# Optimization experiments

Hardware: AMD Instinct MI355X
Metric: run time of the kernel (lower is better)

## Reference

```python
import jax, jax.numpy as jnp
import numpy as np
from jax import lax

LAYER_NUM = 6
EPS = 1e-9
BN_EPS = 1e-5

# CNOT ring on 3 qubits: CNOT(0,1), CNOT(1,2), CNOT(2,0); qubit 0 = MSB.
_P = np.zeros((8, 8), np.float32)
for _b in range(8):
    b0, b1, b2 = (_b >> 2) & 1, (_b >> 1) & 1, _b & 1
    b1 ^= b0
    b2 ^= b1
    b0 ^= b2
    _P[(b0 << 2) | (b1 << 1) | b2, _b] = 1.0
CNOT_RING = jnp.asarray(_P)


def _ry(t):
    c, s = jnp.cos(t / 2), jnp.sin(t / 2)
    return jnp.stack([jnp.stack([c, -s]), jnp.stack([s, c])])


def _channel_unitary(wc):
    # wc: [layer_num, 3] rotation angles -> full 8x8 circuit unitary (real, RY+CNOT)
    U = jnp.eye(8, dtype=wc.dtype)
    for l in range(wc.shape[0]):
        K = jnp.kron(jnp.kron(_ry(wc[l, 0]), _ry(wc[l, 1])), _ry(wc[l, 2]))
        U = CNOT_RING @ K @ U
    return U


def qcnn(x, weights, out_dim, out_size):
    # x: [B, C, H, W]; weights: [C, layer_num, 3]; 2x2 kernel, stride 2, no padding
    B, C, H, W = x.shape
    OH, OW = H // 2, W // 2
    # im2col: [B, C*4, OH, OW] with feature dim ordered (C, kh, kw)
    patches = lax.conv_general_dilated_patches(x, (2, 2), (2, 2), 'VALID')
    patches = patches.reshape(B, C, 4, OH * OW).transpose(0, 1, 3, 2)  # [B,C,P,4]
    # amplitude embedding on 2 data qubits, ancilla (MSB) in |0>
    nrm = jnp.linalg.norm(patches, axis=-1, keepdims=True)
    amp = patches / jnp.maximum(nrm, EPS)
    psi0 = jnp.pad(amp, ((0, 0), (0, 0), (0, 0), (0, 4)))  # [B,C,P,8]
    U = jax.vmap(_channel_unitary)(weights)  # [C,8,8]
    psi = jnp.einsum('cjk,bcpk->bcpj', U, psi0)
    probs = psi * psi
    data = probs[..., :4]  # post-select ancilla = 0
    data = data / jnp.maximum(data.sum(-1, keepdims=True), EPS)
    return data.reshape(B, out_dim, out_size, out_size)


def batchnorm2d(x, gamma, beta):
    mean = x.mean(axis=(0, 2, 3), keepdims=True)
    var = x.var(axis=(0, 2, 3), keepdims=True)
    xn = (x - mean) * lax.rsqrt(var + BN_EPS)
    return xn * gamma[None, :, None, None] + beta[None, :, None, None]


def setup_inputs() -> dict:
    key = jax.random.key(0)
    ks = jax.random.split(key, 5)
    return {
        'z': jax.random.normal(ks[0], (1024, 256, 4, 4), jnp.float32),
        'w1': jax.random.normal(ks[1], (256, LAYER_NUM, 3), jnp.float32),
        'w2': jax.random.normal(ks[2], (64, LAYER_NUM, 3), jnp.float32),
        'w3': jax.random.normal(ks[3], (16, LAYER_NUM, 3), jnp.float32),
        'w4': jax.random.normal(ks[4], (4, LAYER_NUM, 3), jnp.float32),
        'gamma2': jnp.ones((64,), jnp.float32), 'beta2': jnp.zeros((64,), jnp.float32),
        'gamma3': jnp.ones((16,), jnp.float32), 'beta3': jnp.zeros((16,), jnp.float32),
        'gamma4': jnp.ones((4,), jnp.float32), 'beta4': jnp.zeros((4,), jnp.float32),
        'gamma_f': jnp.ones((1,), jnp.float32), 'beta_f': jnp.zeros((1,), jnp.float32),
    }


def reference(z, w1, w2, w3, w4, gamma2, beta2, gamma3, beta3, gamma4, beta4, gamma_f, beta_f):
    s1 = qcnn(z, w1, 64, 8)
    x = jax.nn.relu(batchnorm2d(s1, gamma2, beta2))
    s2 = qcnn(x, w2, 16, 16)
    x = jax.nn.relu(batchnorm2d(s2, gamma3, beta3))
    s3 = qcnn(x, w3, 4, 32)
    x = jax.nn.relu(batchnorm2d(s3, gamma4, beta4))
    s4 = qcnn(x, w4, 1, 64)
    s4_bn = batchnorm2d(s4, gamma_f, beta_f)
    return jnp.tanh(s4_bn), s4, s4_bn
```

## Files before the change

### kernel.cpp

```cpp
#include <hip/hip_runtime.h>
#include <math.h>


#define NB 1024

__global__ __launch_bounds__(256) void build_V_kernel(
    const float* __restrict__ w1, const float* __restrict__ w2,
    const float* __restrict__ w3, const float* __restrict__ w4,
    float* __restrict__ V)
{
    int t = blockIdx.x * blockDim.x + threadIdx.x;
    if (t >= 340) return;
    const float* w; float* vout;
    if (t < 256)      { w = w1 + t*18;        vout = V + t*16; }
    else if (t < 320) { w = w2 + (t-256)*18;  vout = V + 4096 + (t-256)*16; }
    else if (t < 336) { w = w3 + (t-320)*18;  vout = V + 5120 + (t-320)*16; }
    else              { w = w4 + (t-336)*18;  vout = V + 5376 + (t-336)*16; }
    const int perm[8] = {0,5,7,2,3,6,4,1};
    float U[8][8];
    #pragma unroll
    for (int i=0;i<8;i++)
        #pragma unroll
        for (int j=0;j<8;j++) U[i][j] = (i==j) ? 1.0f : 0.0f;
    for (int l=0;l<6;l++){
        float c0 = cosf(0.5f*w[l*3+0]), s0 = sinf(0.5f*w[l*3+0]);
        float c1 = cosf(0.5f*w[l*3+1]), s1 = sinf(0.5f*w[l*3+1]);
        float c2 = cosf(0.5f*w[l*3+2]), s2 = sinf(0.5f*w[l*3+2]);
        #pragma unroll
        for (int col=0; col<8; col++){
            float v[8];
            #pragma unroll
            for (int r=0;r<8;r++) v[r] = U[r][col];
            #pragma unroll
            for (int b=0;b<8;b+=2){ float x=v[b], y=v[b+1]; v[b]=c2*x-s2*y; v[b+1]=s2*x+c2*y; }
            #pragma unroll
            for (int g=0;g<8;g+=4)
                #pragma unroll
                for (int i=0;i<2;i++){ int a=g+i, b=g+i+2; float x=v[a], y=v[b]; v[a]=c1*x-s1*y; v[b]=s1*x+c1*y; }
            #pragma unroll
            for (int i=0;i<4;i++){ float x=v[i], y=v[i+4]; v[i]=c0*x-s0*y; v[i+4]=s0*x+c0*y; }
            #pragma unroll
            for (int r=0;r<8;r++) U[perm[r]][col] = v[r];
        }
    }
    #pragma unroll
    for (int j=0;j<4;j++)
        #pragma unroll
        for (int k=0;k<4;k++) vout[j*4+k] = U[j][k];
}

template<int C, int H, int W, bool BN>
__global__ __launch_bounds__(256) void qcnn_kernel(
    const float* __restrict__ x, const float* __restrict__ V,
    const float* __restrict__ scale, const float* __restrict__ shift,
    float* __restrict__ out, float* __restrict__ psum, float* __restrict__ pssq)
{
    constexpr int HW  = H*W;
    constexpr int P   = HW/4;
    constexpr int OW  = W/2;
    constexpr int LP  = (P==4)?2:(P==16)?4:(P==64)?6:8;
    constexpr int LOW = (OW==2)?1:(OW==4)?2:(OW==8)?3:4;
    constexpr int OC  = C/4;
    constexpr int CPB = 256/P;
    constexpr int OCB = (CPB/4) < 1 ? 1 : (CPB/4);
    constexpr int DIV = OC/OCB;
    constexpr int NSLOT = NB/DIV;
    constexpr int G   = (4*P < 64) ? 4*P : 64;

    __shared__ float sBin[2*OCB];
    if (threadIdx.x < 2*OCB) sBin[threadIdx.x] = 0.0f;
    __syncthreads();

    const int r0  = (blockIdx.x & 3) * 256;
    const int oc0 = r0 >> (LP+2);

    for (int it=0; it<4; ++it){
        int tid = (it<<18) + (blockIdx.x<<8) + threadIdx.x;
        int b  = tid >> 10;
        int r  = tid & 1023;
        int c  = r >> LP;
        int p  = r & (P-1);
        int oh = p >> LOW;
        int ow = p & (OW-1);
        const float* xb = x + ((size_t)b<<12) + c*HW + (oh*2)*W + (ow*2);
        float2 t0 = *reinterpret_cast<const float2*>(xb);
        float2 t1 = *reinterpret_cast<const float2*>(xb + W);
        float x0=t0.x, x1=t0.y, x2=t1.x, x3=t1.y;
        if constexpr (BN){
            float sc = scale[c], sh = shift[c];
            x0 = fmaxf(x0*sc+sh, 0.0f);
            x1 = fmaxf(x1*sc+sh, 0.0f);
            x2 = fmaxf(x2*sc+sh, 0.0f);
            x3 = fmaxf(x3*sc+sh, 0.0f);
        }
        float nrm = sqrtf(x0*x0 + x1*x1 + x2*x2 + x3*x3);
        float inv = 1.0f / fmaxf(nrm, 1e-9f);
        float a0=x0*inv, a1=x1*inv, a2=x2*inv, a3=x3*inv;
        const float4* Vc = reinterpret_cast<const float4*>(V + c*16);
        float4 v0 = Vc[0], v1 = Vc[1], v2 = Vc[2], v3 = Vc[3];
        float q0 = v0.x*a0 + v0.y*a1 + v0.z*a2 + v0.w*a3;
        float q1 = v1.x*a0 + v1.y*a1 + v1.z*a2 + v1.w*a3;
        float q2 = v2.x*a0 + v2.y*a1 + v2.z*a2 + v2.w*a3;
        float q3 = v3.x*a0 + v3.y*a1 + v3.z*a2 + v3.w*a3;
        q0*=q0; q1*=q1; q2*=q2; q3*=q3;
        float s = q0+q1+q2+q3;
        float dinv = 1.0f / fmaxf(s, 1e-9f);
        float d0=q0*dinv, d1=q1*dinv, d2=q2*dinv, d3=q3*dinv;
        *reinterpret_cast<float4*>(out + ((size_t)b<<12) + c*HW + (p<<2)) =
            make_float4(d0,d1,d2,d3);
        float ls  = d0+d1+d2+d3;
        float lss = d0*d0 + d1*d1 + d2*d2 + d3*d3;
        #pragma unroll
        for (int off=1; off<G; off<<=1){ ls += __shfl_xor(ls, off); lss += __shfl_xor(lss, off); }
        if ((threadIdx.x & (G-1)) == 0){
            int ocl = (r >> (LP+2)) - oc0;
            atomicAdd(&sBin[ocl], ls);
            atomicAdd(&sBin[OCB + ocl], lss);
        }
    }
    __syncthreads();
    if (threadIdx.x < OCB){
        int slot = blockIdx.x / DIV;
        psum[(oc0 + threadIdx.x)*NSLOT + slot] = sBin[threadIdx.x];
        pssq[(oc0 + threadIdx.x)*NSLOT + slot] = sBin[OCB + threadIdx.x];
    }
}

__global__ __launch_bounds__(256) void stats_kernel(
    const float* __restrict__ psum, const float* __restrict__ pssq,
    const float* __restrict__ gamma, const float* __restrict__ beta,
    float* __restrict__ scale, float* __restrict__ shift,
    int nslot, float invN)
{
    __shared__ float sh[8];
    int oc = blockIdx.x;
    float s=0.0f, ss=0.0f;
    for (int i=threadIdx.x; i<nslot; i+=256){ s += psum[oc*nslot+i]; ss += pssq[oc*nslot+i]; }
    #pragma unroll
    for (int off=32; off; off>>=1){ s += __shfl_down(s, off); ss += __shfl_down(ss, off); }
    int wid = threadIdx.x >> 6, lane = threadIdx.x & 63;
    if (lane==0){ sh[wid]=s; sh[4+wid]=ss; }
    __syncthreads();
    if (threadIdx.x==0){
        s  = sh[0]+sh[1]+sh[2]+sh[3];
        ss = sh[4]+sh[5]+sh[6]+sh[7];
        float mean = s*invN;
        float var  = ss*invN - mean*mean;
        float rinv = 1.0f / sqrtf(var + 1e-5f);
        float sc = gamma[oc]*rinv;
        scale[oc] = sc;
        shift[oc] = beta[oc] - mean*sc;
    }
}

__global__ __launch_bounds__(256) void final_kernel(
    const float* __restrict__ s4, const float* __restrict__ sc_p,
    const float* __restrict__ sh_p, float* __restrict__ out_tanh,
    float* __restrict__ out_bn)
{
    float sc = sc_p[0], sh = sh_p[0];
    int i = blockIdx.x*blockDim.x + threadIdx.x;
    float4 v = reinterpret_cast<const float4*>(s4)[i];
    float4 bn = make_float4(v.x*sc+sh, v.y*sc+sh, v.z*sc+sh, v.w*sc+sh);
    reinterpret_cast<float4*>(out_bn)[i] = bn;
    reinterpret_cast<float4*>(out_tanh)[i] =
        make_float4(tanhf(bn.x), tanhf(bn.y), tanhf(bn.z), tanhf(bn.w));
}

extern "C" void kernel_launch(void* const* d_in, const int* in_sizes, int n_in,
                              void* d_out, int out_size, void* d_ws, size_t ws_size,
                              hipStream_t stream)
{
    const float* z      = (const float*)d_in[0];
    const float* w1     = (const float*)d_in[1];
    const float* w2     = (const float*)d_in[2];
    const float* w3     = (const float*)d_in[3];
    const float* w4     = (const float*)d_in[4];
    const float* gamma2 = (const float*)d_in[5];
    const float* beta2  = (const float*)d_in[6];
    const float* gamma3 = (const float*)d_in[7];
    const float* beta3  = (const float*)d_in[8];
    const float* gamma4 = (const float*)d_in[9];
    const float* beta4  = (const float*)d_in[10];
    const float* gammaf = (const float*)d_in[11];
    const float* betaf  = (const float*)d_in[12];
    float* out = (float*)d_out;
    float* ws  = (float*)d_ws;

    float* V      = ws;
    float* scale2 = ws + 5504;  float* shift2 = ws + 5568;
    float* scale3 = ws + 5632;  float* shift3 = ws + 5696;
    float* scale4 = ws + 5760;  float* shift4 = ws + 5824;
    float* scalef = ws + 5888;  float* shiftf = ws + 5952;
    float* ps1 = ws + 6144;   float* pq1 = ws + 22528;
    float* ps2 = ws + 38912;  float* pq2 = ws + 43008;
    float* ps3 = ws + 47104;  float* pq3 = ws + 48128;
    float* ps4 = ws + 49152;  float* pq4 = ws + 50176;
    float* bufA = ws + 65536;
    float* bufB = ws + 65536 + 4194304;
    float* s4   = out + 4194304;
    float* s4bn = out + 8388608;

    build_V_kernel<<<2, 256, 0, stream>>>(w1, w2, w3, w4, V);

    qcnn_kernel<256,4,4,false><<<NB, 256, 0, stream>>>(z, V, nullptr, nullptr, bufA, ps1, pq1);
    stats_kernel<<<64, 256, 0, stream>>>(ps1, pq1, gamma2, beta2, scale2, shift2, 256, 1.0f/65536.0f);

    qcnn_kernel<64,8,8,true><<<NB, 256, 0, stream>>>(bufA, V+4096, scale2, shift2, bufB, ps2, pq2);
    stats_kernel<<<16, 256, 0, stream>>>(ps2, pq2, gamma3, beta3, scale3, shift3, 256, 1.0f/262144.0f);

    qcnn_kernel<16,16,16,true><<<NB, 256, 0, stream>>>(bufB, V+5120, scale3, shift3, bufA, ps3, pq3);
    stats_kernel<<<4, 256, 0, stream>>>(ps3, pq3, gamma4, beta4, scale4, shift4, 256, 1.0f/1048576.0f);

    qcnn_kernel<4,32,32,true><<<NB, 256, 0, stream>>>(bufA, V+5376, scale4, shift4, s4, ps4, pq4);
    stats_kernel<<<1, 256, 0, stream>>>(ps4, pq4, gammaf, betaf, scalef, shiftf, 1024, 1.0f/4194304.0f);

    final_kernel<<<4096, 256, 0, stream>>>(s4, scalef, shiftf, out, s4bn);
}
```

Measured before the change: 146.9 us.

## Fuse all QCNN layers into one cooperative kernel with per-image LDS residency

Replaces the nine separate layer, stats and final launches with a single cooperative kernel. Each block keeps one 4096-float image in shared memory across all four layers, and grid.sync handles the global batchnorm statistics. Per-block partial sums are reduced with atomics into 8 banked global accumulators instead of slot arrays plus stats kernels. This removes intermediate global round-trips and launch gaps, but adds four grid-wide barriers and needs all 1024 blocks (16KB LDS each) to be co-resident.

```diff
diff --git a/kernel.cpp b/kernel.cpp
--- a/kernel.cpp
+++ b/kernel.cpp
@@ -1,15 +1,18 @@
 #include <hip/hip_runtime.h>
+#include <hip/hip_cooperative_groups.h>
 #include <math.h>
 
-
-#define NB 1024
+namespace cg = cooperative_groups;
+
 
 __global__ __launch_bounds__(256) void build_V_kernel(
     const float* __restrict__ w1, const float* __restrict__ w2,
     const float* __restrict__ w3, const float* __restrict__ w4,
-    float* __restrict__ V)
+    float* __restrict__ V, float* __restrict__ acc)
 {
     int t = blockIdx.x * blockDim.x + threadIdx.x;
+    int j = t - 512;
+    if (j >= 0 && j < 1360) acc[j] = 0.0f;
     if (t >= 340) return;
     const float* w; float* vout;
     if (t < 256)      { w = w1 + t*18;        vout = V + t*16; }
@@ -21,7 +24,7 @@
     #pragma unroll
     for (int i=0;i<8;i++)
         #pragma unroll
-        for (int j=0;j<8;j++) U[i][j] = (i==j) ? 1.0f : 0.0f;
+        for (int jj=0;jj<8;jj++) U[i][jj] = (i==jj) ? 1.0f : 0.0f;
     for (int l=0;l<6;l++){
         float c0 = cosf(0.5f*w[l*3+0]), s0 = sinf(0.5f*w[l*3+0]);
         float c1 = cosf(0.5f*w[l*3+1]), s1 = sinf(0.5f*w[l*3+1]);
@@ -32,11 +35,11 @@
             #pragma unroll
             for (int r=0;r<8;r++) v[r] = U[r][col];
             #pragma unroll
-            for (int b=0;b<8;b+=2){ float x=v[b], y=v[b+1]; v[b]=c2*x-s2*y; v[b+1]=s2*x+c2*y; }
+            for (int bb=0;bb<8;bb+=2){ float x=v[bb], y=v[bb+1]; v[bb]=c2*x-s2*y; v[bb+1]=s2*x+c2*y; }
             #pragma unroll
             for (int g=0;g<8;g+=4)
                 #pragma unroll
-                for (int i=0;i<2;i++){ int a=g+i, b=g+i+2; float x=v[a], y=v[b]; v[a]=c1*x-s1*y; v[b]=s1*x+c1*y; }
+                for (int i=0;i<2;i++){ int a=g+i, bq=g+i+2; float x=v[a], y=v[bq]; v[a]=c1*x-s1*y; v[bq]=s1*x+c1*y; }
             #pragma unroll
             for (int i=0;i<4;i++){ float x=v[i], y=v[i+4]; v[i]=c0*x-s0*y; v[i+4]=s0*x+c0*y; }
             #pragma unroll
@@ -44,127 +47,177 @@
         }
     }
     #pragma unroll
-    for (int j=0;j<4;j++)
-        #pragma unroll
-        for (int k=0;k<4;k++) vout[j*4+k] = U[j][k];
+    for (int jj=0;jj<4;jj++)
+        #pragma unroll
+        for (int k=0;k<4;k++) vout[jj*4+k] = U[jj][k];
 }
 
 template<int C, int H, int W, bool BN>
-__global__ __launch_bounds__(256) void qcnn_kernel(
-    const float* __restrict__ x, const float* __restrict__ V,
-    const float* __restrict__ scale, const float* __restrict__ shift,
-    float* __restrict__ out, float* __restrict__ psum, float* __restrict__ pssq)
+__device__ __forceinline__ void layer_step(
+    float* __restrict__ data, const float* __restrict__ Vg,
+    const float* __restrict__ sSc, const float* __restrict__ sSh,
+    float* __restrict__ sbin, float* __restrict__ accL, int bank,
+    float* __restrict__ gout, int b)
 {
     constexpr int HW  = H*W;
     constexpr int P   = HW/4;
     constexpr int OW  = W/2;
+    constexpr int OC  = C/4;
     constexpr int LP  = (P==4)?2:(P==16)?4:(P==64)?6:8;
     constexpr int LOW = (OW==2)?1:(OW==4)?2:(OW==8)?3:4;
-    constexpr int OC  = C/4;
-    constexpr int CPB = 256/P;
-    constexpr int OCB = (CPB/4) < 1 ? 1 : (CPB/4);
-    constexpr int DIV = OC/OCB;
-    constexpr int NSLOT = NB/DIV;
-    constexpr int G   = (4*P < 64) ? 4*P : 64;
-
-    __shared__ float sBin[2*OCB];
-    if (threadIdx.x < 2*OCB) sBin[threadIdx.x] = 0.0f;
-    __syncthreads();
-
-    const int r0  = (blockIdx.x & 3) * 256;
-    const int oc0 = r0 >> (LP+2);
-
-    for (int it=0; it<4; ++it){
-        int tid = (it<<18) + (blockIdx.x<<8) + threadIdx.x;
-        int b  = tid >> 10;
-        int r  = tid & 1023;
-        int c  = r >> LP;
-        int p  = r & (P-1);
-        int oh = p >> LOW;
-        int ow = p & (OW-1);
-        const float* xb = x + ((size_t)b<<12) + c*HW + (oh*2)*W + (ow*2);
-        float2 t0 = *reinterpret_cast<const float2*>(xb);
-        float2 t1 = *reinterpret_cast<const float2*>(xb + W);
-        float x0=t0.x, x1=t0.y, x2=t1.x, x3=t1.y;
+    constexpr int RED = ((1<<(LP+2)) < 64) ? (1<<(LP+2)) : 64;
+    const int tid = threadIdx.x;
+
+    if (tid < 2*OC) sbin[tid] = 0.0f;
+    __syncthreads();
+
+    float xv[4][4];
+    #pragma unroll
+    for (int k=0;k<4;k++){
+        int u = tid + 256*k;
+        int c = u >> LP, p = u & (P-1);
+        int oh = p >> LOW, ow = p & (OW-1);
+        int base = c*HW + (oh*2)*W + (ow*2);
+        float x0 = data[base], x1 = data[base+1];
+        float x2 = data[base+W], x3 = data[base+W+1];
         if constexpr (BN){
-            float sc = scale[c], sh = shift[c];
-            x0 = fmaxf(x0*sc+sh, 0.0f);
-            x1 = fmaxf(x1*sc+sh, 0.0f);
-            x2 = fmaxf(x2*sc+sh, 0.0f);
-            x3 = fmaxf(x3*sc+sh, 0.0f);
-        }
+            float sc = sSc[c], sh = sSh[c];
+            x0 = fmaxf(fmaf(x0,sc,sh), 0.0f);
+            x1 = fmaxf(fmaf(x1,sc,sh), 0.0f);
+            x2 = fmaxf(fmaf(x2,sc,sh), 0.0f);
+            x3 = fmaxf(fmaf(x3,sc,sh), 0.0f);
+        }
+        xv[k][0]=x0; xv[k][1]=x1; xv[k][2]=x2; xv[k][3]=x3;
+    }
+    __syncthreads();
+
+    #pragma unroll
+    for (int k=0;k<4;k++){
+        int u = tid + 256*k;
+        int c = u >> LP, p = u & (P-1);
+        float x0=xv[k][0], x1=xv[k][1], x2=xv[k][2], x3=xv[k][3];
         float nrm = sqrtf(x0*x0 + x1*x1 + x2*x2 + x3*x3);
         float inv = 1.0f / fmaxf(nrm, 1e-9f);
         float a0=x0*inv, a1=x1*inv, a2=x2*inv, a3=x3*inv;
-        const float4* Vc = reinterpret_cast<const float4*>(V + c*16);
+        const float4* Vc = reinterpret_cast<const float4*>(Vg + (c<<4));
         float4 v0 = Vc[0], v1 = Vc[1], v2 = Vc[2], v3 = Vc[3];
         float q0 = v0.x*a0 + v0.y*a1 + v0.z*a2 + v0.w*a3;
         float q1 = v1.x*a0 + v1.y*a1 + v1.z*a2 + v1.w*a3;
         float q2 = v2.x*a0 + v2.y*a1 + v2.z*a2 + v2.w*a3;
         float q3 = v3.x*a0 + v3.y*a1 + v3.z*a2 + v3.w*a3;
         q0*=q0; q1*=q1; q2*=q2; q3*=q3;
-        float s = q0+q1+q2+q3;
-        float dinv = 1.0f / fmaxf(s, 1e-9f);
+        float dinv = 1.0f / fmaxf(q0+q1+q2+q3, 1e-9f);
         float d0=q0*dinv, d1=q1*dinv, d2=q2*dinv, d3=q3*dinv;
-        *reinterpret_cast<float4*>(out + ((size_t)b<<12) + c*HW + (p<<2)) =
-            make_float4(d0,d1,d2,d3);
+        float4 o4 = make_float4(d0,d1,d2,d3);
+        reinterpret_cast<float4*>(data)[c*P + p] = o4;
+        if (gout)
+            reinterpret_cast<float4*>(gout)[(size_t)b*1024 + u] = o4;
         float ls  = d0+d1+d2+d3;
         float lss = d0*d0 + d1*d1 + d2*d2 + d3*d3;
         #pragma unroll
-        for (int off=1; off<G; off<<=1){ ls += __shfl_xor(ls, off); lss += __shfl_xor(lss, off); }
-        if ((threadIdx.x & (G-1)) == 0){
-            int ocl = (r >> (LP+2)) - oc0;
-            atomicAdd(&sBin[ocl], ls);
-            atomicAdd(&sBin[OCB + ocl], lss);
-        }
-    }
-    __syncthreads();
-    if (threadIdx.x < OCB){
-        int slot = blockIdx.x / DIV;
-        psum[(oc0 + threadIdx.x)*NSLOT + slot] = sBin[threadIdx.x];
-        pssq[(oc0 + threadIdx.x)*NSLOT + slot] = sBin[OCB + threadIdx.x];
-    }
-}
-
-__global__ __launch_bounds__(256) void stats_kernel(
-    const float* __restrict__ psum, const float* __restrict__ pssq,
+        for (int off=1; off<RED; off<<=1){
+            ls  += __shfl_xor(ls,  off);
+            lss += __shfl_xor(lss, off);
+        }
+        if ((tid & (RED-1)) == 0){
+            int oc = u >> (LP+2);
+            atomicAdd(&sbin[oc],      ls);
+            atomicAdd(&sbin[OC + oc], lss);
+        }
+    }
+    __syncthreads();
+
+    if (tid < OC){
+        atomicAdd(&accL[bank*2*OC + tid],      sbin[tid]);
+        atomicAdd(&accL[bank*2*OC + OC + tid], sbin[OC + tid]);
+    }
+}
+
+template<int OC>
+__device__ __forceinline__ void bn_params(
+    const float* __restrict__ accL,
     const float* __restrict__ gamma, const float* __restrict__ beta,
-    float* __restrict__ scale, float* __restrict__ shift,
-    int nslot, float invN)
-{
-    __shared__ float sh[8];
-    int oc = blockIdx.x;
-    float s=0.0f, ss=0.0f;
-    for (int i=threadIdx.x; i<nslot; i+=256){ s += psum[oc*nslot+i]; ss += pssq[oc*nslot+i]; }
-    #pragma unroll
-    for (int off=32; off; off>>=1){ s += __shfl_down(s, off); ss += __shfl_down(ss, off); }
-    int wid = threadIdx.x >> 6, lane = threadIdx.x & 63;
-    if (lane==0){ sh[wid]=s; sh[4+wid]=ss; }
-    __syncthreads();
-    if (threadIdx.x==0){
-        s  = sh[0]+sh[1]+sh[2]+sh[3];
-        ss = sh[4]+sh[5]+sh[6]+sh[7];
+    float invN, float* __restrict__ sSc, float* __restrict__ sSh, int tid)
+{
+    if (tid < OC){
+        float s=0.0f, q=0.0f;
+        #pragma unroll
+        for (int bk=0;bk<8;bk++){
+            s += accL[bk*2*OC + tid];
+            q += accL[bk*2*OC + OC + tid];
+        }
         float mean = s*invN;
-        float var  = ss*invN - mean*mean;
-        float rinv = 1.0f / sqrtf(var + 1e-5f);
-        float sc = gamma[oc]*rinv;
-        scale[oc] = sc;
-        shift[oc] = beta[oc] - mean*sc;
-    }
-}
-
-__global__ __launch_bounds__(256) void final_kernel(
-    const float* __restrict__ s4, const float* __restrict__ sc_p,
-    const float* __restrict__ sh_p, float* __restrict__ out_tanh,
+        float var  = q*invN - mean*mean;
+        float r    = 1.0f / sqrtf(var + 1e-5f);
+        float sc   = gamma[tid]*r;
+        sSc[tid] = sc;
+        sSh[tid] = beta[tid] - mean*sc;
+    }
+    __syncthreads();
+}
+
+__global__ __launch_bounds__(256, 4) void fused_kernel(
+    const float* __restrict__ z, const float* __restrict__ V,
+    float* __restrict__ acc,
+    const float* __restrict__ g2, const float* __restrict__ b2,
+    const float* __restrict__ g3, const float* __restrict__ b3,
+    const float* __restrict__ g4, const float* __restrict__ b4,
+    const float* __restrict__ gf, const float* __restrict__ bf,
+    float* __restrict__ out_tanh, float* __restrict__ out_s4,
     float* __restrict__ out_bn)
 {
-    float sc = sc_p[0], sh = sh_p[0];
-    int i = blockIdx.x*blockDim.x + threadIdx.x;
-    float4 v = reinterpret_cast<const float4*>(s4)[i];
-    float4 bn = make_float4(v.x*sc+sh, v.y*sc+sh, v.z*sc+sh, v.w*sc+sh);
-    reinterpret_cast<float4*>(out_bn)[i] = bn;
-    reinterpret_cast<float4*>(out_tanh)[i] =
-        make_float4(tanhf(bn.x), tanhf(bn.y), tanhf(bn.z), tanhf(bn.w));
+    __shared__ __align__(16) float data[4096];
+    __shared__ float sbin[128];
+    __shared__ float sSc[64], sSh[64];
+    const int tid  = threadIdx.x;
+    const int b    = blockIdx.x;
+    const int bank = b & 7;
+    cg::grid_group grid = cg::this_grid();
+
+    float* acc1 = acc;
+    float* acc2 = acc + 1024;
+    float* acc3 = acc + 1280;
+    float* acc4 = acc + 1344;
+
+    const float4* zb = reinterpret_cast<const float4*>(z) + (size_t)b*1024;
+    float4* dv = reinterpret_cast<float4*>(data);
+    #pragma unroll
+    for (int k=0;k<4;k++) dv[k*256+tid] = zb[k*256+tid];
+
+    layer_step<256,4,4,false>(data, V,      nullptr, nullptr, sbin, acc1, bank, nullptr, b);
+    grid.sync();
+    bn_params<64>(acc1, g2, b2, 1.0f/65536.0f,   sSc, sSh, tid);
+
+    layer_step<64,8,8,true>(data, V+4096, sSc, sSh, sbin, acc2, bank, nullptr, b);
+    grid.sync();
+    bn_params<16>(acc2, g3, b3, 1.0f/262144.0f,  sSc, sSh, tid);
+
+    layer_step<16,16,16,true>(data, V+5120, sSc, sSh, sbin, acc3, bank, nullptr, b);
+    grid.sync();
+    bn_params<4>(acc3, g4, b4, 1.0f/1048576.0f,  sSc, sSh, tid);
+
+    layer_step<4,32,32,true>(data, V+5376, sSc, sSh, sbin, acc4, bank, out_s4, b);
+    grid.sync();
+
+    float s=0.0f, q=0.0f;
+    #pragma unroll
+    for (int bk=0;bk<8;bk++){ s += acc4[bk*2]; q += acc4[bk*2+1]; }
+    float mean = s*(1.0f/4194304.0f);
+    float var  = q*(1.0f/4194304.0f) - mean*mean;
+    float r    = 1.0f / sqrtf(var + 1e-5f);
+    float sc   = gf[0]*r;
+    float sh   = bf[0] - mean*sc;
+    float4* ot = reinterpret_cast<float4*>(out_tanh) + (size_t)b*1024;
+    float4* ob = reinterpret_cast<float4*>(out_bn)   + (size_t)b*1024;
+    #pragma unroll
+    for (int k=0;k<4;k++){
+        float4 v = dv[k*256+tid];
+        float4 bnv = make_float4(fmaf(v.x,sc,sh), fmaf(v.y,sc,sh),
+                                 fmaf(v.z,sc,sh), fmaf(v.w,sc,sh));
+        ob[k*256+tid] = bnv;
+        ot[k*256+tid] = make_float4(tanhf(bnv.x), tanhf(bnv.y),
+                                    tanhf(bnv.z), tanhf(bnv.w));
+    }
 }
 
 extern "C" void kernel_launch(void* const* d_in, const int* in_sizes, int n_in,
@@ -187,33 +240,23 @@
     float* out = (float*)d_out;
     float* ws  = (float*)d_ws;
 
-    float* V      = ws;
-    float* scale2 = ws + 5504;  float* shift2 = ws + 5568;
-    float* scale3 = ws + 5632;  float* shift3 = ws + 5696;
-    float* scale4 = ws + 5760;  float* shift4 = ws + 5824;
-    float* scalef = ws + 5888;  float* shiftf = ws + 5952;
-    float* ps1 = ws + 6144;   float* pq1 = ws + 22528;
-    float* ps2 = ws + 38912;  float* pq2 = ws + 43008;
-    float* ps3 = ws + 47104;  float* pq3 = ws + 48128;
-    float* ps4 = ws + 49152;  float* pq4 = ws + 50176;
-    float* bufA = ws + 65536;
-    float* bufB = ws + 65536 + 4194304;
-    float* s4   = out + 4194304;
-    float* s4bn = out + 8388608;
-
-    build_V_kernel<<<2, 256, 0, stream>>>(w1, w2, w3, w4, V);
-
-    qcnn_kernel<256,4,4,false><<<NB, 256, 0, stream>>>(z, V, nullptr, nullptr, bufA, ps1, pq1);
-    stats_kernel<<<64, 256, 0, stream>>>(ps1, pq1, gamma2, beta2, scale2, shift2, 256, 1.0f/65536.0f);
-
-    qcnn_kernel<64,8,8,true><<<NB, 256, 0, stream>>>(bufA, V+4096, scale2, shift2, bufB, ps2, pq2);
-    stats_kernel<<<16, 256, 0, stream>>>(ps2, pq2, gamma3, beta3, scale3, shift3, 256, 1.0f/262144.0f);
-
-    qcnn_kernel<16,16,16,true><<<NB, 256, 0, stream>>>(bufB, V+5120, scale3, shift3, bufA, ps3, pq3);
-    stats_kernel<<<4, 256, 0, stream>>>(ps3, pq3, gamma4, beta4, scale4, shift4, 256, 1.0f/1048576.0f);
-
-    qcnn_kernel<4,32,32,true><<<NB, 256, 0, stream>>>(bufA, V+5376, scale4, shift4, s4, ps4, pq4);
-    stats_kernel<<<1, 256, 0, stream>>>(ps4, pq4, gammaf, betaf, scalef, shiftf, 1024, 1.0f/4194304.0f);
-
-    final_kernel<<<4096, 256, 0, stream>>>(s4, scalef, shiftf, out, s4bn);
-}
+    float* V   = ws;
+    float* acc = ws + 8192;
+
+    float* out_tanh = out;
+    float* out_s4   = out + 4194304;
+    float* out_bn   = out + 8388608;
+
+    build_V_kernel<<<8, 256, 0, stream>>>(w1, w2, w3, w4, V, acc);
+
+    void* args[] = {
+        (void*)&z, (void*)&V, (void*)&acc,
+        (void*)&gamma2, (void*)&beta2,
+        (void*)&gamma3, (void*)&beta3,
+        (void*)&gamma4, (void*)&beta4,
+        (void*)&gammaf, (void*)&betaf,
+        (void*)&out_tanh, (void*)&out_s4, (void*)&out_bn
+    };
+    hipLaunchCooperativeKernel((const void*)fused_kernel,
+                               dim3(1024), dim3(256), args, 0, stream);
+}
```

Result: slower. 576.1 us (+292.1%).

## Fuse BN stats reduction into qcnn kernels via banked global atomics

Applied to the files above, without the earlier changes.

Removes the four separate stats kernels. Each qcnn block now atomically adds its per-channel partial sums into one of 8 global banks. The next layer's kernel reduces the banks and computes BN scale and shift into shared memory in its prologue, and the final kernel does the same for the last layer. This cuts four kernel launches and the partial-buffer traffic, at the cost of global atomics and redundant per-block stats computation. The accumulators are zeroed in build_V, so build_V must launch with enough blocks to cover them.

```diff
diff --git a/kernel.cpp b/kernel.cpp
--- a/kernel.cpp
+++ b/kernel.cpp
@@ -7,9 +7,11 @@
 __global__ __launch_bounds__(256) void build_V_kernel(
     const float* __restrict__ w1, const float* __restrict__ w2,
     const float* __restrict__ w3, const float* __restrict__ w4,
-    float* __restrict__ V)
+    float* __restrict__ V, float* __restrict__ acc)
 {
     int t = blockIdx.x * blockDim.x + threadIdx.x;
+    int j = t - 512;
+    if (j >= 0 && j < 1360) acc[j] = 0.0f;
     if (t >= 340) return;
     const float* w; float* vout;
     if (t < 256)      { w = w1 + t*18;        vout = V + t*16; }
@@ -21,7 +23,7 @@
     #pragma unroll
     for (int i=0;i<8;i++)
         #pragma unroll
-        for (int j=0;j<8;j++) U[i][j] = (i==j) ? 1.0f : 0.0f;
+        for (int jj=0;jj<8;jj++) U[i][jj] = (i==jj) ? 1.0f : 0.0f;
     for (int l=0;l<6;l++){
         float c0 = cosf(0.5f*w[l*3+0]), s0 = sinf(0.5f*w[l*3+0]);
         float c1 = cosf(0.5f*w[l*3+1]), s1 = sinf(0.5f*w[l*3+1]);
@@ -32,11 +34,11 @@
             #pragma unroll
             for (int r=0;r<8;r++) v[r] = U[r][col];
             #pragma unroll
-            for (int b=0;b<8;b+=2){ float x=v[b], y=v[b+1]; v[b]=c2*x-s2*y; v[b+1]=s2*x+c2*y; }
+            for (int bb=0;bb<8;bb+=2){ float x=v[bb], y=v[bb+1]; v[bb]=c2*x-s2*y; v[bb+1]=s2*x+c2*y; }
             #pragma unroll
             for (int g=0;g<8;g+=4)
                 #pragma unroll
-                for (int i=0;i<2;i++){ int a=g+i, b=g+i+2; float x=v[a], y=v[b]; v[a]=c1*x-s1*y; v[b]=s1*x+c1*y; }
+                for (int i=0;i<2;i++){ int a=g+i, bq=g+i+2; float x=v[a], y=v[bq]; v[a]=c1*x-s1*y; v[bq]=s1*x+c1*y; }
             #pragma unroll
             for (int i=0;i<4;i++){ float x=v[i], y=v[i+4]; v[i]=c0*x-s0*y; v[i+4]=s0*x+c0*y; }
             #pragma unroll
@@ -44,16 +46,17 @@
         }
     }
     #pragma unroll
-    for (int j=0;j<4;j++)
-        #pragma unroll
-        for (int k=0;k<4;k++) vout[j*4+k] = U[j][k];
+    for (int jj=0;jj<4;jj++)
+        #pragma unroll
+        for (int k=0;k<4;k++) vout[jj*4+k] = U[jj][k];
 }
 
 template<int C, int H, int W, bool BN>
 __global__ __launch_bounds__(256) void qcnn_kernel(
     const float* __restrict__ x, const float* __restrict__ V,
-    const float* __restrict__ scale, const float* __restrict__ shift,
-    float* __restrict__ out, float* __restrict__ psum, float* __restrict__ pssq)
+    const float* __restrict__ accPrev, const float* __restrict__ gamma,
+    const float* __restrict__ beta, float invN,
+    float* __restrict__ out, float* __restrict__ accOut)
 {
     constexpr int HW  = H*W;
     constexpr int P   = HW/4;
@@ -61,23 +64,39 @@
     constexpr int LP  = (P==4)?2:(P==16)?4:(P==64)?6:8;
     constexpr int LOW = (OW==2)?1:(OW==4)?2:(OW==8)?3:4;
     constexpr int OC  = C/4;
-    constexpr int CPB = 256/P;
-    constexpr int OCB = (CPB/4) < 1 ? 1 : (CPB/4);
-    constexpr int DIV = OC/OCB;
-    constexpr int NSLOT = NB/DIV;
+    constexpr int OCB = (64/P) < 1 ? 1 : (64/P);
     constexpr int G   = (4*P < 64) ? 4*P : 64;
 
     __shared__ float sBin[2*OCB];
-    if (threadIdx.x < 2*OCB) sBin[threadIdx.x] = 0.0f;
+    __shared__ float sSc[C], sSh[C];
+    const int tid = threadIdx.x;
+
+    if (tid < 2*OCB) sBin[tid] = 0.0f;
+    if constexpr (BN){
+        if (tid < C){
+            float s=0.0f, q=0.0f;
+            #pragma unroll
+            for (int bk=0;bk<8;bk++){
+                s += accPrev[bk*2*C + tid];
+                q += accPrev[bk*2*C + C + tid];
+            }
+            float mean = s*invN;
+            float var  = q*invN - mean*mean;
+            float r    = 1.0f / sqrtf(var + 1e-5f);
+            float sc   = gamma[tid]*r;
+            sSc[tid] = sc;
+            sSh[tid] = beta[tid] - mean*sc;
+        }
+    }
     __syncthreads();
 
     const int r0  = (blockIdx.x & 3) * 256;
     const int oc0 = r0 >> (LP+2);
 
     for (int it=0; it<4; ++it){
-        int tid = (it<<18) + (blockIdx.x<<8) + threadIdx.x;
-        int b  = tid >> 10;
-        int r  = tid & 1023;
+        int tg = (it<<18) + (blockIdx.x<<8) + tid;
+        int b  = tg >> 10;
+        int r  = tg & 1023;
         int c  = r >> LP;
         int p  = r & (P-1);
         int oh = p >> LOW;
@@ -87,81 +106,70 @@
         float2 t1 = *reinterpret_cast<const float2*>(xb + W);
         float x0=t0.x, x1=t0.y, x2=t1.x, x3=t1.y;
         if constexpr (BN){
-            float sc = scale[c], sh = shift[c];
-            x0 = fmaxf(x0*sc+sh, 0.0f);
-            x1 = fmaxf(x1*sc+sh, 0.0f);
-            x2 = fmaxf(x2*sc+sh, 0.0f);
-            x3 = fmaxf(x3*sc+sh, 0.0f);
+            float sc = sSc[c], sh = sSh[c];
+            x0 = fmaxf(fmaf(x0,sc,sh), 0.0f);
+            x1 = fmaxf(fmaf(x1,sc,sh), 0.0f);
+            x2 = fmaxf(fmaf(x2,sc,sh), 0.0f);
+            x3 = fmaxf(fmaf(x3,sc,sh), 0.0f);
         }
         float nrm = sqrtf(x0*x0 + x1*x1 + x2*x2 + x3*x3);
         float inv = 1.0f / fmaxf(nrm, 1e-9f);
         float a0=x0*inv, a1=x1*inv, a2=x2*inv, a3=x3*inv;
-        const float4* Vc = reinterpret_cast<const float4*>(V + c*16);
+        const float4* Vc = reinterpret_cast<const float4*>(V + (c<<4));
         float4 v0 = Vc[0], v1 = Vc[1], v2 = Vc[2], v3 = Vc[3];
         float q0 = v0.x*a0 + v0.y*a1 + v0.z*a2 + v0.w*a3;
         float q1 = v1.x*a0 + v1.y*a1 + v1.z*a2 + v1.w*a3;
         float q2 = v2.x*a0 + v2.y*a1 + v2.z*a2 + v2.w*a3;
         float q3 = v3.x*a0 + v3.y*a1 + v3.z*a2 + v3.w*a3;
         q0*=q0; q1*=q1; q2*=q2; q3*=q3;
-        float s = q0+q1+q2+q3;
-        float dinv = 1.0f / fmaxf(s, 1e-9f);
+        float dinv = 1.0f / fmaxf(q0+q1+q2+q3, 1e-9f);
         float d0=q0*dinv, d1=q1*dinv, d2=q2*dinv, d3=q3*dinv;
-        *reinterpret_cast<float4*>(out + ((size_t)b<<12) + c*HW + (p<<2)) =
+        *reinterpret_cast<float4*>(out + ((size_t)b<<12) + (r<<2)) =
             make_float4(d0,d1,d2,d3);
         float ls  = d0+d1+d2+d3;
         float lss = d0*d0 + d1*d1 + d2*d2 + d3*d3;
         #pragma unroll
-        for (int off=1; off<G; off<<=1){ ls += __shfl_xor(ls, off); lss += __shfl_xor(lss, off); }
-        if ((threadIdx.x & (G-1)) == 0){
+        for (int off=1; off<G; off<<=1){
+            ls  += __shfl_xor(ls,  off);
+            lss += __shfl_xor(lss, off);
+        }
+        if ((tid & (G-1)) == 0){
             int ocl = (r >> (LP+2)) - oc0;
             atomicAdd(&sBin[ocl], ls);
             atomicAdd(&sBin[OCB + ocl], lss);
         }
     }
     __syncthreads();
-    if (threadIdx.x < OCB){
-        int slot = blockIdx.x / DIV;
-        psum[(oc0 + threadIdx.x)*NSLOT + slot] = sBin[threadIdx.x];
-        pssq[(oc0 + threadIdx.x)*NSLOT + slot] = sBin[OCB + threadIdx.x];
-    }
-}
-
-__global__ __launch_bounds__(256) void stats_kernel(
-    const float* __restrict__ psum, const float* __restrict__ pssq,
-    const float* __restrict__ gamma, const float* __restrict__ beta,
-    float* __restrict__ scale, float* __restrict__ shift,
-    int nslot, float invN)
-{
-    __shared__ float sh[8];
-    int oc = blockIdx.x;
-    float s=0.0f, ss=0.0f;
-    for (int i=threadIdx.x; i<nslot; i+=256){ s += psum[oc*nslot+i]; ss += pssq[oc*nslot+i]; }
-    #pragma unroll
-    for (int off=32; off; off>>=1){ s += __shfl_down(s, off); ss += __shfl_down(ss, off); }
-    int wid = threadIdx.x >> 6, lane = threadIdx.x & 63;
-    if (lane==0){ sh[wid]=s; sh[4+wid]=ss; }
+    if (tid < OCB){
+        int bank = blockIdx.x & 7;
+        atomicAdd(&accOut[bank*2*OC + oc0 + tid],      sBin[tid]);
+        atomicAdd(&accOut[bank*2*OC + OC + oc0 + tid], sBin[OCB + tid]);
+    }
+}
+
+__global__ __launch_bounds__(256) void final_kernel(
+    const float* __restrict__ s4, const float* __restrict__ acc4,
+    const float* __restrict__ gf, const float* __restrict__ bf,
+    float* __restrict__ out_tanh, float* __restrict__ out_bn)
+{
+    __shared__ float sP[2];
+    if (threadIdx.x == 0){
+        float s=0.0f, q=0.0f;
+        #pragma unroll
+        for (int bk=0;bk<8;bk++){ s += acc4[bk*2]; q += acc4[bk*2+1]; }
+        float mean = s*(1.0f/4194304.0f);
+        float var  = q*(1.0f/4194304.0f) - mean*mean;
+        float r    = 1.0f / sqrtf(var + 1e-5f);
+        float sc   = gf[0]*r;
+        sP[0] = sc;
+        sP[1] = bf[0] - mean*sc;
+    }
     __syncthreads();
-    if (threadIdx.x==0){
-        s  = sh[0]+sh[1]+sh[2]+sh[3];
-        ss = sh[4]+sh[5]+sh[6]+sh[7];
-        float mean = s*invN;
-        float var  = ss*invN - mean*mean;
-        float rinv = 1.0f / sqrtf(var + 1e-5f);
-        float sc = gamma[oc]*rinv;
-        scale[oc] = sc;
-        shift[oc] = beta[oc] - mean*sc;
-    }
-}
-
-__global__ __launch_bounds__(256) void final_kernel(
-    const float* __restrict__ s4, const float* __restrict__ sc_p,
-    const float* __restrict__ sh_p, float* __restrict__ out_tanh,
-    float* __restrict__ out_bn)
-{
-    float sc = sc_p[0], sh = sh_p[0];
+    float sc = sP[0], sh = sP[1];
     int i = blockIdx.x*blockDim.x + threadIdx.x;
     float4 v = reinterpret_cast<const float4*>(s4)[i];
-    float4 bn = make_float4(v.x*sc+sh, v.y*sc+sh, v.z*sc+sh, v.w*sc+sh);
+    float4 bn = make_float4(fmaf(v.x,sc,sh), fmaf(v.y,sc,sh),
+                            fmaf(v.z,sc,sh), fmaf(v.w,sc,sh));
     reinterpret_cast<float4*>(out_bn)[i] = bn;
     reinterpret_cast<float4*>(out_tanh)[i] =
         make_float4(tanhf(bn.x), tanhf(bn.y), tanhf(bn.z), tanhf(bn.w));
@@ -187,33 +195,29 @@
     float* out = (float*)d_out;
     float* ws  = (float*)d_ws;
 
-    float* V      = ws;
-    float* scale2 = ws + 5504;  float* shift2 = ws + 5568;
-    float* scale3 = ws + 5632;  float* shift3 = ws + 5696;
-    float* scale4 = ws + 5760;  float* shift4 = ws + 5824;
-    float* scalef = ws + 5888;  float* shiftf = ws + 5952;
-    float* ps1 = ws + 6144;   float* pq1 = ws + 22528;
-    float* ps2 = ws + 38912;  float* pq2 = ws + 43008;
-    float* ps3 = ws + 47104;  float* pq3 = ws + 48128;
-    float* ps4 = ws + 49152;  float* pq4 = ws + 50176;
-    float* bufA = ws + 65536;
-    float* bufB = ws + 65536 + 4194304;
-    float* s4   = out + 4194304;
-    float* s4bn = out + 8388608;
-
-    build_V_kernel<<<2, 256, 0, stream>>>(w1, w2, w3, w4, V);
-
-    qcnn_kernel<256,4,4,false><<<NB, 256, 0, stream>>>(z, V, nullptr, nullptr, bufA, ps1, pq1);
-    stats_kernel<<<64, 256, 0, stream>>>(ps1, pq1, gamma2, beta2, scale2, shift2, 256, 1.0f/65536.0f);
-
-    qcnn_kernel<64,8,8,true><<<NB, 256, 0, stream>>>(bufA, V+4096, scale2, shift2, bufB, ps2, pq2);
-    stats_kernel<<<16, 256, 0, stream>>>(ps2, pq2, gamma3, beta3, scale3, shift3, 256, 1.0f/262144.0f);
-
-    qcnn_kernel<16,16,16,true><<<NB, 256, 0, stream>>>(bufB, V+5120, scale3, shift3, bufA, ps3, pq3);
-    stats_kernel<<<4, 256, 0, stream>>>(ps3, pq3, gamma4, beta4, scale4, shift4, 256, 1.0f/1048576.0f);
-
-    qcnn_kernel<4,32,32,true><<<NB, 256, 0, stream>>>(bufA, V+5376, scale4, shift4, s4, ps4, pq4);
-    stats_kernel<<<1, 256, 0, stream>>>(ps4, pq4, gammaf, betaf, scalef, shiftf, 1024, 1.0f/4194304.0f);
-
-    final_kernel<<<4096, 256, 0, stream>>>(s4, scalef, shiftf, out, s4bn);
-}
+    float* V    = ws;
+    float* acc  = ws + 8192;
+    float* acc1 = acc;
+    float* acc2 = acc + 1024;
+    float* acc3 = acc + 1280;
+    float* acc4 = acc + 1344;
+    float* bufA = ws + 16384;
+    float* bufB = ws + 16384 + 4194304;
+
+    float* out_tanh = out;
+    float* s4       = out + 4194304;
+    float* out_bn   = out + 8388608;
+
+    build_V_kernel<<<8, 256, 0, stream>>>(w1, w2, w3, w4, V, acc);
+
+    qcnn_kernel<256,4,4,false><<<NB, 256, 0, stream>>>(
+        z, V, nullptr, nullptr, nullptr, 0.0f, bufA, acc1);
+    qcnn_kernel<64,8,8,true><<<NB, 256, 0, stream>>>(
+        bufA, V+4096, acc1, gamma2, beta2, 1.0f/65536.0f, bufB, acc2);
+    qcnn_kernel<16,16,16,true><<<NB, 256, 0, stream>>>(
+        bufB, V+5120, acc2, gamma3, beta3, 1.0f/262144.0f, bufA, acc3);
+    qcnn_kernel<4,32,32,true><<<NB, 256, 0, stream>>>(
+        bufA, V+5376, acc3, gamma4, beta4, 1.0f/1048576.0f, s4, acc4);
+    final_kernel<<<4096, 256, 0, stream>>>(
+        s4, acc4, gammaf, betaf, out_tanh, out_bn);
+}
```

Result: slower. 176.0 us (+19.8%).
